# Performance work log

Hardware: AMD Instinct MI355X
Metric: run time of the kernel (lower is better)

The kernel has to match this reference:

```python
import jax, jax.numpy as jnp
import numpy as np

N = 1024      # num_waves
L = 32        # latent_dim
H = 64        # hidden_dim
EPS = 1e-6
SELF_SCALE = 0.5
INT_SCALE = 0.3


def _xavier(k, shape, gain=0.5):
    fan_out, fan_in = shape
    std = gain * np.sqrt(2.0 / (fan_in + fan_out))
    return (jax.random.normal(k, shape, jnp.float32) * std).astype(jnp.float32)


def setup_inputs() -> dict:
    key = jax.random.key(0)
    ks = jax.random.split(key, 12)
    d = {}
    d['state'] = jax.random.normal(ks[0], (N * (L + 1),), jnp.float32)
    # SelfDynamicsNetwork: L->H->H->L, tanh, xavier_normal gain=0.5, zero bias
    d['Ws1'] = _xavier(ks[1], (H, L)); d['bs1'] = jnp.zeros((H,), jnp.float32)
    d['Ws2'] = _xavier(ks[2], (H, H)); d['bs2'] = jnp.zeros((H,), jnp.float32)
    d['Ws3'] = _xavier(ks[3], (L, H)); d['bs3'] = jnp.zeros((L,), jnp.float32)
    # InteractionNetwork: 4L->H->H->L
    d['Wi1'] = _xavier(ks[4], (H, 4 * L)); d['bi1'] = jnp.zeros((H,), jnp.float32)
    d['Wi2'] = _xavier(ks[5], (H, H));     d['bi2'] = jnp.zeros((H,), jnp.float32)
    d['Wi3'] = _xavier(ks[6], (L, H));     d['bi3'] = jnp.zeros((L,), jnp.float32)
    # QuantumPhaseMixer
    d['phase_w'] = jax.random.normal(ks[7], (L,), jnp.float32) * 0.1
    d['Wc'] = _xavier(ks[8], (L, 2 * L), gain=1.0)
    d['bc'] = jnp.zeros((L,), jnp.float32)
    # per-wave aggressiveness
    d['aggr'] = jnp.ones((N,), jnp.float32) * 0.5
    return d


def reference(state, Ws1, bs1, Ws2, bs2, Ws3, bs3,
              Wi1, bi1, Wi2, bi2, Wi3, bi3,
              phase_w, Wc, bc, aggr):
    s = state.reshape(N, L + 1)
    h = s[:, :L]          # [N, L]
    phases = s[:, L]      # [N]

    def mlp(x, W1, b1, W2, b2, W3, b3):
        x = jnp.tanh(x @ W1.T + b1)
        x = jnp.tanh(x @ W2.T + b2)
        return x @ W3.T + b3

    self_term = mlp(h, Ws1, bs1, Ws2, bs2, Ws3, bs3)   # [N, L]
    dh = self_term  # prev_state is None -> estimated velocity = self_dynamics(h)

    # pairwise distance factor
    diff = h[:, None, :] - h[None, :, :]                # [N, N, L] (h_i - h_j)
    dist = jnp.linalg.norm(diff, axis=-1) + EPS         # [N, N]
    dfac = jnp.minimum(1.0 / dist, 2.0)

    # InteractionNetwork on concat([h_i, h_j, dh_i, dh_j]): split first layer
    a_i = h @ Wi1[:, :L].T + dh @ Wi1[:, 2 * L:3 * L].T           # [N, H]
    b_j = h @ Wi1[:, L:2 * L].T + dh @ Wi1[:, 3 * L:].T + bi1    # [N, H]
    x1 = jnp.tanh(a_i[:, None, :] + b_j[None, :, :])              # [N, N, H]
    x2 = jnp.tanh(x1 @ Wi2.T + bi2)                               # [N, N, H]
    k_ij = x2 @ Wi3.T + bi3                                       # [N, N, L]

    # QuantumPhaseMixer
    phase_diff = phases[:, None] - phases[None, :]                # [N, N]
    pf = jnp.cos(phase_diff[..., None] * phase_w)                 # [N, N, L]
    coh = jax.nn.sigmoid((h @ Wc[:, :L].T)[:, None, :]
                         + (h @ Wc[:, L:].T)[None, :, :] + bc)    # [N, N, L]
    quantum = pf * coh * (-diff)                                  # h_j - h_i = -diff

    agg = jax.nn.sigmoid(aggr)                                    # [N]
    inter = dfac[..., None] * k_ij * agg[:, None, None] + quantum # [N, N, L]
    mask = 1.0 - jnp.eye(N, dtype=inter.dtype)                    # skip j == i
    isum = jnp.einsum('ijl,ij->il', inter, mask)                  # sum over j

    # env is None -> speed_mults = 1, refractions = 0
    dh_dt = SELF_SCALE * self_term + INT_SCALE * isum
    dphase = 0.1 + 0.05 * jnp.sum(jnp.abs(isum), axis=-1)
    return jnp.concatenate([dh_dt, dphase[:, None]], axis=1).reshape(-1)
```

## Files before the change

kernel.cpp:

```cpp
#include <hip/hip_runtime.h>
#include <hip/hip_bf16.h>
#include <math.h>

#define NN 1024
#define LDIM 32
#define HDIM 64

#define WS_SELF 0
#define WS_AA   (WS_SELF + NN*LDIM)
#define WS_CI   (WS_AA   + NN*HDIM)
#define WS_AGG  (WS_CI   + NN*LDIM)
#define WS_BI2  (WS_AGG  + NN)
#define WS_BI3  (WS_BI2  + HDIM)
#define WS_BCB  (WS_BI3  + LDIM)
#define WS_FEND (WS_BCB  + LDIM)

#define U_BJB  0
#define U_HJB  (U_BJB + NN*HDIM)
#define U_JT   (U_HJB + NN*LDIM)
#define U_W2B  (U_JT  + NN*LDIM*4)
#define U_W3B  (U_W2B + HDIM*HDIM)
#define U_END  (U_W3B + LDIM*HDIM)

#define PK_W1  0
#define PK_W2  1024
#define PK_W3  3072
#define PK_WI1 4096
#define PK_WC  8192
#define PK_END 9216

typedef __attribute__((ext_vector_type(8))) short bf16x8;
typedef __attribute__((ext_vector_type(4))) float f32x4;

__device__ __forceinline__ float fast_rcp(float x) { return __builtin_amdgcn_rcpf(x); }
__device__ __forceinline__ float fast_tanh(float x) {
    float e = __builtin_amdgcn_exp2f(x * 2.88539008f);
    return 1.0f - 2.0f * fast_rcp(e + 1.0f);
}
__device__ __forceinline__ float fast_sigmoid(float x) {
    return fast_rcp(1.0f + __builtin_amdgcn_exp2f(x * -1.44269504f));
}
__device__ __forceinline__ float blo(unsigned int u) { union { unsigned int i; float f; } v; v.i = u << 16; return v.f; }
__device__ __forceinline__ float bhi(unsigned int u) { union { unsigned int i; float f; } v; v.i = u & 0xffff0000u; return v.f; }
__device__ __forceinline__ float bf2f(unsigned short u) { union { unsigned int i; float f; } v; v.i = ((unsigned int)u) << 16; return v.f; }
__device__ __forceinline__ unsigned short f2bf(float f) {
    __hip_bfloat16 b = __float2bfloat16(f);
    unsigned short u; __builtin_memcpy(&u, &b, 2); return u;
}
__device__ __forceinline__ unsigned int pk2(float a, float b) {
    float2 t; t.x = a; t.y = b;
    __hip_bfloat162 h = __float22bfloat162_rn(t);
    unsigned int u; __builtin_memcpy(&u, &h, 4); return u;
}

__global__ __launch_bounds__(256) void precompute(
    const float* __restrict__ state,
    const float* __restrict__ Ws1, const float* __restrict__ bs1,
    const float* __restrict__ Ws2, const float* __restrict__ bs2,
    const float* __restrict__ Ws3, const float* __restrict__ bs3,
    const float* __restrict__ Wi1, const float* __restrict__ bi1,
    const float* __restrict__ Wi2, const float* __restrict__ bi2,
    const float* __restrict__ Wi3, const float* __restrict__ bi3,
    const float* __restrict__ phw, const float* __restrict__ Wc,
    const float* __restrict__ bc,  const float* __restrict__ aggr,
    float* __restrict__ ws, unsigned short* __restrict__ wsu) {
    const int tid = threadIdx.x;
    const int w = tid >> 6, t = tid & 63;
    const int i = blockIdx.x * 4 + w;

    __shared__ unsigned int wlds[PK_END];
    __shared__ float shh[4][32], shdh[4][32], sht1[4][64], sht2[4][64];
    __shared__ float shph[4];

    {
        const float2* s1 = (const float2*)Ws1;
        #pragma unroll
        for (int r = 0; r < 4; r++) { int e = tid + r * 256; int f = e >> 4, k2 = e & 15;
            float2 v = s1[e]; wlds[PK_W1 + k2 * 64 + f] = pk2(v.x, v.y); }
        const float2* s2 = (const float2*)Ws2;
        #pragma unroll
        for (int r = 0; r < 8; r++) { int e = tid + r * 256; int f = e >> 5, k2 = e & 31;
            float2 v = s2[e]; wlds[PK_W2 + k2 * 64 + f] = pk2(v.x, v.y); }
        const float2* s3 = (const float2*)Ws3;
        #pragma unroll
        for (int r = 0; r < 4; r++) { int e = tid + r * 256; int f = e >> 5, k2 = e & 31;
            float2 v = s3[e]; wlds[PK_W3 + k2 * 32 + f] = pk2(v.x, v.y); }
        const float2* si = (const float2*)Wi1;
        #pragma unroll
        for (int r = 0; r < 16; r++) { int e = tid + r * 256; int f = e >> 6, c2 = e & 63;
            float2 v = si[e]; wlds[PK_WI1 + c2 * 64 + f] = pk2(v.x, v.y); }
        const float2* sc = (const float2*)Wc;
        #pragma unroll
        for (int r = 0; r < 4; r++) { int e = tid + r * 256; int f = e >> 5, c2 = e & 31;
            float2 v = sc[e]; wlds[PK_WC + c2 * 32 + f] = pk2(v.x, v.y); }
    }
    if (blockIdx.x == 0) {
        #pragma unroll
        for (int r = 0; r < 16; r++) { int e = tid + r * 256; wsu[U_W2B + e] = f2bf(Wi2[e]); }
        #pragma unroll
        for (int r = 0; r < 8; r++)  { int e = tid + r * 256; wsu[U_W3B + e] = f2bf(Wi3[e]); }
        if (tid < HDIM) ws[WS_BI2 + tid] = bi2[tid];
        if (tid < LDIM) { ws[WS_BI3 + tid] = bi3[tid]; ws[WS_BCB + tid] = bc[tid]; }
    }

    float sv = (t < 33) ? state[i * 33 + t] : 0.f;
    if (t < 32) shh[w][t] = sv;
    if (t == 32) shph[w] = sv;
    if (t == 33) ws[WS_AGG + i] = fast_sigmoid(aggr[i]);
    __syncthreads();

    {
        float s = bs1[t];
        const unsigned int* W = wlds + PK_W1;
        #pragma unroll
        for (int k2 = 0; k2 < 16; k2++) {
            unsigned int p = W[k2 * 64 + t];
            s = fmaf(blo(p), shh[w][2 * k2], s);
            s = fmaf(bhi(p), shh[w][2 * k2 + 1], s);
        }
        sht1[w][t] = fast_tanh(s);
    }
    __syncthreads();
    {
        float s = bs2[t];
        const unsigned int* W = wlds + PK_W2;
        #pragma unroll
        for (int k2 = 0; k2 < 32; k2++) {
            unsigned int p = W[k2 * 64 + t];
            s = fmaf(blo(p), sht1[w][2 * k2], s);
            s = fmaf(bhi(p), sht1[w][2 * k2 + 1], s);
        }
        sht2[w][t] = fast_tanh(s);
    }
    __syncthreads();
    if (t < 32) {
        float s = bs3[t];
        const unsigned int* W = wlds + PK_W3;
        #pragma unroll
        for (int k2 = 0; k2 < 32; k2++) {
            unsigned int p = W[k2 * 32 + t];
            s = fmaf(blo(p), sht2[w][2 * k2], s);
            s = fmaf(bhi(p), sht2[w][2 * k2 + 1], s);
        }
        ws[WS_SELF + i * 32 + t] = s;
        shdh[w][t] = s;
    }
    __syncthreads();
    {
        float sa = 0.f, sb = bi1[t];
        const unsigned int* W = wlds + PK_WI1;
        #pragma unroll
        for (int k2 = 0; k2 < 16; k2++) {
            float h0 = shh[w][2 * k2], h1 = shh[w][2 * k2 + 1];
            float d0 = shdh[w][2 * k2], d1 = shdh[w][2 * k2 + 1];
            unsigned int wa  = W[k2 * 64 + t];
            unsigned int wb  = W[(16 + k2) * 64 + t];
            unsigned int wa2 = W[(32 + k2) * 64 + t];
            unsigned int wb2 = W[(48 + k2) * 64 + t];
            sa = fmaf(blo(wa), h0, sa);  sa = fmaf(bhi(wa), h1, sa);
            sb = fmaf(blo(wb), h0, sb);  sb = fmaf(bhi(wb), h1, sb);
            sa = fmaf(blo(wa2), d0, sa); sa = fmaf(bhi(wa2), d1, sa);
            sb = fmaf(blo(wb2), d0, sb); sb = fmaf(bhi(wb2), d1, sb);
        }
        ws[WS_AA + i * 64 + t] = sa;
        wsu[U_BJB + i * 64 + t] = f2bf(sb);
    }
    if (t < 32) {
        float si = 0.f, sj = 0.f;
        const unsigned int* W = wlds + PK_WC;
        #pragma unroll
        for (int m2 = 0; m2 < 16; m2++) {
            float h0 = shh[w][2 * m2], h1 = shh[w][2 * m2 + 1];
            unsigned int wi = W[m2 * 32 + t];
            unsigned int wj = W[(16 + m2) * 32 + t];
            si = fmaf(blo(wi), h0, si); si = fmaf(bhi(wi), h1, si);
            sj = fmaf(blo(wj), h0, sj); sj = fmaf(bhi(wj), h1, sj);
        }
        ws[WS_CI + i * 32 + t] = si;
        float h = shh[w][t];
        wsu[U_HJB + i * 32 + t] = f2bf(h);
        float sc, cc;
        __sincosf(shph[w] * phw[t], &sc, &cc);
        uint2 jt; jt.x = pk2(h, sj); jt.y = pk2(cc, sc);
        *(uint2*)(wsu + U_JT + (i * 32 + t) * 4) = jt;
    }
}

__global__ __launch_bounds__(256) void pair_kernel(
    const float* __restrict__ ws, const unsigned short* __restrict__ wsu,
    float* __restrict__ out) {
    const int i    = blockIdx.x;
    const int tid  = threadIdx.x;
    const int w    = tid >> 6;
    const int lane = tid & 63;
    const int q    = lane >> 4;
    const int m    = lane & 15;
    const int jw   = w * 16;
    const int sub  = lane & 3;

    __shared__ unsigned short W2ls[64 * 72];
    __shared__ unsigned short W3ls[32 * 72];
    __shared__ unsigned short x2ls[4 * 16 * 72];
    __shared__ float aLS[64];
    __shared__ float red[4][32];

    if (tid < 64) aLS[tid] = ws[WS_AA + i * 64 + tid];
    {
        int row = tid >> 2, c = (tid & 3) * 16;
        const uint4* s2 = (const uint4*)(wsu + U_W2B + row * 64 + c);
        uint4 d0 = s2[0], d1 = s2[1];
        uint4* dd = (uint4*)(&W2ls[row * 72 + c]);
        dd[0] = d0; dd[1] = d1;
        if (row < 32) {
            const uint4* s3 = (const uint4*)(wsu + U_W3B + row * 64 + c);
            uint4 e0 = s3[0], e1 = s3[1];
            uint4* d3 = (uint4*)(&W3ls[row * 72 + c]);
            d3[0] = e0; d3[1] = e1;
        }
    }
    float hi8[8];
    {
        uint4 hv4 = *(const uint4*)(wsu + U_HJB + i * 32 + sub * 8);
        unsigned int hd[4] = {hv4.x, hv4.y, hv4.z, hv4.w};
        #pragma unroll
        for (int e = 0; e < 4; e++) { hi8[2 * e] = blo(hd[e]); hi8[2 * e + 1] = bhi(hd[e]); }
    }
    float bi2v[4];
    #pragma unroll
    for (int nb = 0; nb < 4; nb++) bi2v[nb] = ws[WS_BI2 + nb * 16 + m];
    float hiv[2], cibv[2], picv[2], pisv[2], bi3v[2];
    #pragma unroll
    for (int lb = 0; lb < 2; lb++) {
        int l = lb * 16 + m;
        uint2 jti = *(const uint2*)(wsu + U_JT + (i * 32 + l) * 4);
        hiv[lb] = blo(jti.x);
        picv[lb] = blo(jti.y); pisv[lb] = bhi(jti.y);
        cibv[lb] = ws[WS_CI + i * 32 + l] + ws[WS_BCB + l];
        bi3v[lb] = ws[WS_BI3 + l];
    }
    const float aggi = ws[WS_AGG + i];

    const unsigned short* hp = wsu + U_HJB + (jw + (lane >> 2)) * 32 + sub * 8;
    const unsigned short* bp = wsu + U_BJB + (jw + m) * 64 + q * 8;
    const unsigned short* jp = wsu + U_JT + ((jw + q * 4) * 32 + m) * 4;

    uint4 hv = *(const uint4*)hp;
    uint4 bv0 = *(const uint4*)bp;
    uint4 bv1 = *(const uint4*)(bp + 32);
    uint2 jt0[4], jt1[4];
    #pragma unroll
    for (int r = 0; r < 4; r++) {
        jt0[r] = *(const uint2*)(jp + r * 128);
        jt1[r] = *(const uint2*)(jp + 64 + r * 128);
    }
    __syncthreads();

    float accC0 = 0.f, accC1 = 0.f;

    for (int T = 0; T < 16; T++) {
        const int jb = T * 64;
        uint4 hvc = hv, bv0c = bv0, bv1c = bv1;
        uint2 jc0[4], jc1[4];
        #pragma unroll
        for (int r = 0; r < 4; r++) { jc0[r] = jt0[r]; jc1[r] = jt1[r]; }
        if (T < 15) {
            hp += 2048; bp += 4096; jp += 8192;
            hv = *(const uint4*)hp;
            bv0 = *(const uint4*)bp;
            bv1 = *(const uint4*)(bp + 32);
            #pragma unroll
            for (int r = 0; r < 4; r++) {
                jt0[r] = *(const uint2*)(jp + r * 128);
                jt1[r] = *(const uint2*)(jp + 64 + r * 128);
            }
        }

        float fv[4];
        {
            unsigned int hd[4] = {hvc.x, hvc.y, hvc.z, hvc.w};
            float s = 0.f;
            #pragma unroll
            for (int e = 0; e < 4; e++) {
                float d0 = hi8[2 * e]     - blo(hd[e]);
                float d1 = hi8[2 * e + 1] - bhi(hd[e]);
                s = fmaf(d0, d0, s); s = fmaf(d1, d1, s);
            }
            s += __shfl_xor(s, 1); s += __shfl_xor(s, 2);
            float facown = fminf(fast_rcp(sqrtf(s) + 1e-6f), 2.0f) * aggi;
            #pragma unroll
            for (int r = 0; r < 4; r++) fv[r] = __shfl(facown, (q * 4 + r) * 4);
        }

        bf16x8 afrag[2];
        {
            unsigned int bd[8] = {bv0c.x, bv0c.y, bv0c.z, bv0c.w, bv1c.x, bv1c.y, bv1c.z, bv1c.w};
            #pragma unroll
            for (int s = 0; s < 2; s++) {
                union { uint4 u4; bf16x8 v; } pkd;
                #pragma unroll
                for (int e = 0; e < 4; e++) {
                    const float* ab = &aLS[s * 32 + q * 8 + 2 * e];
                    float x0 = fast_tanh(ab[0] + blo(bd[s * 4 + e]));
                    float x1 = fast_tanh(ab[1] + bhi(bd[s * 4 + e]));
                    ((unsigned int*)&pkd.u4)[e] = pk2(x0, x1);
                }
                afrag[s] = pkd.v;
            }
        }

        f32x4 accA[4];
        #pragma unroll
        for (int nb = 0; nb < 4; nb++) {
            f32x4 acc = {0.f, 0.f, 0.f, 0.f};
            #pragma unroll
            for (int s = 0; s < 2; s++) {
                bf16x8 bfrag = *(const bf16x8*)(&W2ls[(nb * 16 + m) * 72 + s * 32 + q * 8]);
                acc = __builtin_amdgcn_mfma_f32_16x16x32_bf16(afrag[s], bfrag, acc, 0, 0, 0);
            }
            accA[nb] = acc;
        }
        {
            unsigned short* xw = &x2ls[w * 16 * 72];
            #pragma unroll
            for (int nb = 0; nb < 4; nb++) {
                #pragma unroll
                for (int r = 0; r < 4; r++)
                    xw[(q * 4 + r) * 72 + nb * 16 + m] = f2bf(fast_tanh(accA[nb][r] + bi2v[nb]));
            }
        }

        f32x4 accB[2];
        {
            bf16x8 x2f[2];
            #pragma unroll
            for (int s = 0; s < 2; s++)
                x2f[s] = *(const bf16x8*)(&x2ls[(w * 16 + m) * 72 + s * 32 + q * 8]);
            #pragma unroll
            for (int lb = 0; lb < 2; lb++) {
                f32x4 acc = {0.f, 0.f, 0.f, 0.f};
                #pragma unroll
                for (int s = 0; s < 2; s++) {
                    bf16x8 w3frag = *(const bf16x8*)(&W3ls[(lb * 16 + m) * 72 + s * 32 + q * 8]);
                    acc = __builtin_amdgcn_mfma_f32_16x16x32_bf16(x2f[s], w3frag, acc, 0, 0, 0);
                }
                accB[lb] = acc;
            }
        }

        #pragma unroll
        for (int lb = 0; lb < 2; lb++) {
            float accl = 0.f;
            #pragma unroll
            for (int r = 0; r < 4; r++) {
                uint2 jv = (lb == 0) ? jc0[r] : jc1[r];
                float hj = blo(jv.x), cj = bhi(jv.x);
                float pjc = blo(jv.y), pjs = bhi(jv.y);
                float pf  = picv[lb] * pjc + pisv[lb] * pjs;
                float coh = fast_sigmoid(cibv[lb] + cj);
                float kv  = accB[lb][r] + bi3v[lb];
                float v   = fv[r] * kv - pf * coh * (hiv[lb] - hj);
                int j = jb + jw + q * 4 + r;
                if (j != i) accl += v;
            }
            if (lb == 0) accC0 += accl; else accC1 += accl;
        }
    }

    accC0 += __shfl_xor(accC0, 16); accC0 += __shfl_xor(accC0, 32);
    accC1 += __shfl_xor(accC1, 16); accC1 += __shfl_xor(accC1, 32);
    if (lane < 16) { red[w][m] = accC0; red[w][16 + m] = accC1; }
    __syncthreads();
    if (tid < 32) {
        float isum = red[0][tid] + red[1][tid] + red[2][tid] + red[3][tid];
        out[i * 33 + tid] = 0.5f * ws[WS_SELF + i * 32 + tid] + 0.3f * isum;
        red[0][tid] = fabsf(isum);
    }
    __syncthreads();
    if (tid == 0) {
        float s = 0.f;
        #pragma unroll
        for (int l = 0; l < 32; l++) s += red[0][l];
        out[i * 33 + 32] = 0.1f + 0.05f * s;
    }
}

extern "C" void kernel_launch(void* const* d_in, const int* in_sizes, int n_in,
                              void* d_out, int out_size, void* d_ws, size_t ws_size,
                              hipStream_t stream) {
    const float* state   = (const float*)d_in[0];
    const float* Ws1     = (const float*)d_in[1];
    const float* bs1     = (const float*)d_in[2];
    const float* Ws2     = (const float*)d_in[3];
    const float* bs2     = (const float*)d_in[4];
    const float* Ws3     = (const float*)d_in[5];
    const float* bs3     = (const float*)d_in[6];
    const float* Wi1     = (const float*)d_in[7];
    const float* bi1     = (const float*)d_in[8];
    const float* Wi2     = (const float*)d_in[9];
    const float* bi2     = (const float*)d_in[10];
    const float* Wi3     = (const float*)d_in[11];
    const float* bi3     = (const float*)d_in[12];
    const float* phase_w = (const float*)d_in[13];
    const float* Wc      = (const float*)d_in[14];
    const float* bc      = (const float*)d_in[15];
    const float* aggr    = (const float*)d_in[16];

    float* ws = (float*)d_ws;
    unsigned short* wsu = (unsigned short*)(ws + WS_FEND);
    float* out = (float*)d_out;

    precompute<<<256, 256, 0, stream>>>(state, Ws1, bs1, Ws2, bs2, Ws3, bs3,
                                        Wi1, bi1, Wi2, bi2, Wi3, bi3,
                                        phase_w, Wc, bc, aggr, ws, wsu);
    pair_kernel<<<NN, 256, 0, stream>>>(ws, wsu, out);
}
```

Measured before the change: 163.9 us.

## Factor distance scale and phase terms out of the inner j loop

The distance factor is folded into the x2 activations before the third-layer MFMA, so the MFMA accumulates directly across j tiles. The bias term bi3 is applied once at the end via the sum of factors, and the cos-difference phase term is split into separate cos/sin sums combined after the loop. The diagonal mask becomes a zeroed factor. Together this moves per-element work out of the hot loop and removes the per-tile accumulator epilogue. It also swaps the MFMA operand order to avoid a transpose, and software-pipelines prefetches with a 2x unrolled lambda. The risk is extra bf16 rounding, since the factor is multiplied in before the bf16 conversion.

```diff
diff --git a/kernel.cpp b/kernel.cpp
--- a/kernel.cpp
+++ b/kernel.cpp
@@ -202,7 +202,8 @@
     __shared__ unsigned short W3ls[32 * 72];
     __shared__ unsigned short x2ls[4 * 16 * 72];
     __shared__ float aLS[64];
-    __shared__ float red[4][32];
+    __shared__ float redT[4][32], redU[4][32], redV[4][32];
+    __shared__ float sfw[4];
 
     if (tid < 64) aLS[tid] = ws[WS_AA + i * 64 + tid];
     {
@@ -225,57 +226,55 @@
         #pragma unroll
         for (int e = 0; e < 4; e++) { hi8[2 * e] = blo(hd[e]); hi8[2 * e + 1] = bhi(hd[e]); }
     }
-    float bi2v[4];
+    f32x4 b2q[4];
     #pragma unroll
-    for (int nb = 0; nb < 4; nb++) bi2v[nb] = ws[WS_BI2 + nb * 16 + m];
-    float hiv[2], cibv[2], picv[2], pisv[2], bi3v[2];
+    for (int nb = 0; nb < 4; nb++) {
+        float4 bv = *(const float4*)(ws + WS_BI2 + nb * 16 + q * 4);
+        b2q[nb][0] = bv.x; b2q[nb][1] = bv.y; b2q[nb][2] = bv.z; b2q[nb][3] = bv.w;
+    }
+    float hiv[2], cibv[2];
     #pragma unroll
     for (int lb = 0; lb < 2; lb++) {
         int l = lb * 16 + m;
-        uint2 jti = *(const uint2*)(wsu + U_JT + (i * 32 + l) * 4);
-        hiv[lb] = blo(jti.x);
-        picv[lb] = blo(jti.y); pisv[lb] = bhi(jti.y);
+        hiv[lb]  = bf2f(wsu[U_HJB + i * 32 + l]);
         cibv[lb] = ws[WS_CI + i * 32 + l] + ws[WS_BCB + l];
-        bi3v[lb] = ws[WS_BI3 + l];
     }
     const float aggi = ws[WS_AGG + i];
+    const float sub0 = (sub == 0) ? 1.0f : 0.0f;
 
     const unsigned short* hp = wsu + U_HJB + (jw + (lane >> 2)) * 32 + sub * 8;
     const unsigned short* bp = wsu + U_BJB + (jw + m) * 64 + q * 8;
     const unsigned short* jp = wsu + U_JT + ((jw + q * 4) * 32 + m) * 4;
 
-    uint4 hv = *(const uint4*)hp;
-    uint4 bv0 = *(const uint4*)bp;
-    uint4 bv1 = *(const uint4*)(bp + 32);
-    uint2 jt0[4], jt1[4];
+    uint4 hvA = *(const uint4*)hp;
+    uint4 b0A = *(const uint4*)bp;
+    uint4 b1A = *(const uint4*)(bp + 32);
+    uint4 hvB, b0B, b1B;
+    __syncthreads();
+
+    f32x4 accK[2];
     #pragma unroll
-    for (int r = 0; r < 4; r++) {
-        jt0[r] = *(const uint2*)(jp + r * 128);
-        jt1[r] = *(const uint2*)(jp + 64 + r * 128);
-    }
-    __syncthreads();
-
-    float accC0 = 0.f, accC1 = 0.f;
-
-    for (int T = 0; T < 16; T++) {
-        const int jb = T * 64;
-        uint4 hvc = hv, bv0c = bv0, bv1c = bv1;
-        uint2 jc0[4], jc1[4];
-        #pragma unroll
-        for (int r = 0; r < 4; r++) { jc0[r] = jt0[r]; jc1[r] = jt1[r]; }
-        if (T < 15) {
-            hp += 2048; bp += 4096; jp += 8192;
-            hv = *(const uint4*)hp;
-            bv0 = *(const uint4*)bp;
-            bv1 = *(const uint4*)(bp + 32);
-            #pragma unroll
-            for (int r = 0; r < 4; r++) {
-                jt0[r] = *(const uint2*)(jp + r * 128);
-                jt1[r] = *(const uint2*)(jp + 64 + r * 128);
-            }
-        }
-
-        float fv[4];
+    for (int lb = 0; lb < 2; lb++) { accK[lb][0]=0.f; accK[lb][1]=0.f; accK[lb][2]=0.f; accK[lb][3]=0.f; }
+    float aU[2] = {0.f, 0.f}, aV[2] = {0.f, 0.f};
+    float sumfac = 0.f;
+
+    unsigned short* xw = &x2ls[w * 16 * 72];
+
+    auto body = [&](int T, uint4 hvc, uint4 b0c, uint4 b1c,
+                    uint4& hvn, uint4& b0n, uint4& b1n) {
+        hp += 2048; bp += 4096;
+        hvn = *(const uint4*)hp;
+        b0n = *(const uint4*)bp;
+        b1n = *(const uint4*)(bp + 32);
+        uint2 jt[8];
+        #pragma unroll
+        for (int r = 0; r < 4; r++) {
+            jt[r]     = *(const uint2*)(jp + r * 128);
+            jt[4 + r] = *(const uint2*)(jp + 64 + r * 128);
+        }
+        jp += 8192;
+
+        float facm;
         {
             unsigned int hd[4] = {hvc.x, hvc.y, hvc.z, hvc.w};
             float s = 0.f;
@@ -286,14 +285,16 @@
                 s = fmaf(d0, d0, s); s = fmaf(d1, d1, s);
             }
             s += __shfl_xor(s, 1); s += __shfl_xor(s, 2);
+            int jj = T * 64 + jw + (lane >> 2);
             float facown = fminf(fast_rcp(sqrtf(s) + 1e-6f), 2.0f) * aggi;
-            #pragma unroll
-            for (int r = 0; r < 4; r++) fv[r] = __shfl(facown, (q * 4 + r) * 4);
-        }
-
-        bf16x8 afrag[2];
+            facown = (jj == i) ? 0.0f : facown;
+            sumfac = fmaf(sub0, facown, sumfac);
+            facm = __shfl(facown, 4 * m);
+        }
+
+        bf16x8 afr[2];
         {
-            unsigned int bd[8] = {bv0c.x, bv0c.y, bv0c.z, bv0c.w, bv1c.x, bv1c.y, bv1c.z, bv1c.w};
+            unsigned int bd[8] = {b0c.x, b0c.y, b0c.z, b0c.w, b1c.x, b1c.y, b1c.z, b1c.w};
             #pragma unroll
             for (int s = 0; s < 2; s++) {
                 union { uint4 u4; bf16x8 v; } pkd;
@@ -304,82 +305,104 @@
                     float x1 = fast_tanh(ab[1] + bhi(bd[s * 4 + e]));
                     ((unsigned int*)&pkd.u4)[e] = pk2(x0, x1);
                 }
-                afrag[s] = pkd.v;
+                afr[s] = pkd.v;
             }
         }
 
         f32x4 accA[4];
         #pragma unroll
         for (int nb = 0; nb < 4; nb++) {
-            f32x4 acc = {0.f, 0.f, 0.f, 0.f};
+            f32x4 acc = b2q[nb];
             #pragma unroll
             for (int s = 0; s < 2; s++) {
-                bf16x8 bfrag = *(const bf16x8*)(&W2ls[(nb * 16 + m) * 72 + s * 32 + q * 8]);
-                acc = __builtin_amdgcn_mfma_f32_16x16x32_bf16(afrag[s], bfrag, acc, 0, 0, 0);
+                bf16x8 w2f = *(const bf16x8*)(&W2ls[(nb * 16 + m) * 72 + s * 32 + q * 8]);
+                acc = __builtin_amdgcn_mfma_f32_16x16x32_bf16(w2f, afr[s], acc, 0, 0, 0);
             }
             accA[nb] = acc;
         }
-        {
-            unsigned short* xw = &x2ls[w * 16 * 72];
-            #pragma unroll
-            for (int nb = 0; nb < 4; nb++) {
-                #pragma unroll
-                for (int r = 0; r < 4; r++)
-                    xw[(q * 4 + r) * 72 + nb * 16 + m] = f2bf(fast_tanh(accA[nb][r] + bi2v[nb]));
-            }
-        }
-
-        f32x4 accB[2];
+        #pragma unroll
+        for (int nb = 0; nb < 4; nb++) {
+            float t0 = fast_tanh(accA[nb][0]) * facm;
+            float t1 = fast_tanh(accA[nb][1]) * facm;
+            float t2 = fast_tanh(accA[nb][2]) * facm;
+            float t3 = fast_tanh(accA[nb][3]) * facm;
+            uint2 pk; pk.x = pk2(t0, t1); pk.y = pk2(t2, t3);
+            *(uint2*)(&xw[m * 72 + nb * 16 + q * 4]) = pk;
+        }
+
         {
             bf16x8 x2f[2];
             #pragma unroll
             for (int s = 0; s < 2; s++)
-                x2f[s] = *(const bf16x8*)(&x2ls[(w * 16 + m) * 72 + s * 32 + q * 8]);
+                x2f[s] = *(const bf16x8*)(&xw[m * 72 + s * 32 + q * 8]);
             #pragma unroll
             for (int lb = 0; lb < 2; lb++) {
-                f32x4 acc = {0.f, 0.f, 0.f, 0.f};
                 #pragma unroll
                 for (int s = 0; s < 2; s++) {
-                    bf16x8 w3frag = *(const bf16x8*)(&W3ls[(lb * 16 + m) * 72 + s * 32 + q * 8]);
-                    acc = __builtin_amdgcn_mfma_f32_16x16x32_bf16(x2f[s], w3frag, acc, 0, 0, 0);
+                    bf16x8 w3f = *(const bf16x8*)(&W3ls[(lb * 16 + m) * 72 + s * 32 + q * 8]);
+                    accK[lb] = __builtin_amdgcn_mfma_f32_16x16x32_bf16(x2f[s], w3f, accK[lb], 0, 0, 0);
                 }
-                accB[lb] = acc;
             }
         }
 
         #pragma unroll
         for (int lb = 0; lb < 2; lb++) {
-            float accl = 0.f;
+            float u = 0.f, v = 0.f;
             #pragma unroll
             for (int r = 0; r < 4; r++) {
-                uint2 jv = (lb == 0) ? jc0[r] : jc1[r];
+                uint2 jv = jt[lb * 4 + r];
                 float hj = blo(jv.x), cj = bhi(jv.x);
                 float pjc = blo(jv.y), pjs = bhi(jv.y);
-                float pf  = picv[lb] * pjc + pisv[lb] * pjs;
                 float coh = fast_sigmoid(cibv[lb] + cj);
-                float kv  = accB[lb][r] + bi3v[lb];
-                float v   = fv[r] * kv - pf * coh * (hiv[lb] - hj);
-                int j = jb + jw + q * 4 + r;
-                if (j != i) accl += v;
+                float cd  = coh * (hiv[lb] - hj);
+                u = fmaf(cd, pjc, u);
+                v = fmaf(cd, pjs, v);
             }
-            if (lb == 0) accC0 += accl; else accC1 += accl;
-        }
-    }
-
-    accC0 += __shfl_xor(accC0, 16); accC0 += __shfl_xor(accC0, 32);
-    accC1 += __shfl_xor(accC1, 16); accC1 += __shfl_xor(accC1, 32);
-    if (lane < 16) { red[w][m] = accC0; red[w][16 + m] = accC1; }
+            aU[lb] += u; aV[lb] += v;
+        }
+    };
+
+    #pragma unroll 1
+    for (int T = 0; T < 16; T += 2) {
+        body(T,     hvA, b0A, b1A, hvB, b0B, b1B);
+        body(T + 1, hvB, b0B, b1B, hvA, b0A, b1A);
+    }
+
+    float T1[2];
+    #pragma unroll
+    for (int lb = 0; lb < 2; lb++) {
+        T1[lb] = (accK[lb][0] + accK[lb][1]) + (accK[lb][2] + accK[lb][3]);
+        T1[lb] += __shfl_xor(T1[lb], 16); T1[lb] += __shfl_xor(T1[lb], 32);
+        aU[lb] += __shfl_xor(aU[lb], 16); aU[lb] += __shfl_xor(aU[lb], 32);
+        aV[lb] += __shfl_xor(aV[lb], 16); aV[lb] += __shfl_xor(aV[lb], 32);
+    }
+    sumfac += __shfl_xor(sumfac, 1);  sumfac += __shfl_xor(sumfac, 2);
+    sumfac += __shfl_xor(sumfac, 4);  sumfac += __shfl_xor(sumfac, 8);
+    sumfac += __shfl_xor(sumfac, 16); sumfac += __shfl_xor(sumfac, 32);
+    if (lane < 16) {
+        redT[w][m] = T1[0];      redT[w][16 + m] = T1[1];
+        redU[w][m] = aU[0];      redU[w][16 + m] = aU[1];
+        redV[w][m] = aV[0];      redV[w][16 + m] = aV[1];
+    }
+    if (lane == 0) sfw[w] = sumfac;
     __syncthreads();
     if (tid < 32) {
-        float isum = red[0][tid] + red[1][tid] + red[2][tid] + red[3][tid];
-        out[i * 33 + tid] = 0.5f * ws[WS_SELF + i * 32 + tid] + 0.3f * isum;
-        red[0][tid] = fabsf(isum);
+        int l = tid;
+        float t1 = (redT[0][l] + redT[1][l]) + (redT[2][l] + redT[3][l]);
+        float uu = (redU[0][l] + redU[1][l]) + (redU[2][l] + redU[3][l]);
+        float vv = (redV[0][l] + redV[1][l]) + (redV[2][l] + redV[3][l]);
+        float sf = (sfw[0] + sfw[1]) + (sfw[2] + sfw[3]);
+        uint2 jti = *(const uint2*)(wsu + U_JT + (i * 32 + l) * 4);
+        float pic = blo(jti.y), pis = bhi(jti.y);
+        float isum = t1 + sf * ws[WS_BI3 + l] - (pic * uu + pis * vv);
+        out[i * 33 + l] = 0.5f * ws[WS_SELF + i * 32 + l] + 0.3f * isum;
+        redT[0][l] = fabsf(isum);
     }
     __syncthreads();
     if (tid == 0) {
         float s = 0.f;
         #pragma unroll
-        for (int l = 0; l < 32; l++) s += red[0][l];
+        for (int l = 0; l < 32; l++) s += redT[0][l];
         out[i * 33 + 32] = 0.1f + 0.05f * s;
     }
 }
```

New measurement: 154.6 us. 1.06x faster.
